# Kernel optimization log

Measured on AMD Instinct MI355X. Metric: run time of the kernel, lower is better.

## Reference

```python
import jax, jax.numpy as jnp
import numpy as np

RADIUS = float(1.5 * 6 * 0.025 / 2.0)  # filter_extent / 2 = 0.1125
N_FLUID, N_BOX, K_F, K_B = 16000, 8000, 64, 32
KS = 4  # kernel size per axis -> 64 bins
EPS = 1e-12


def _radius_neighbors(q, p, radius, K, exclude_self=False):
    Nq = q.shape[0]
    idx = np.zeros((Nq, K), np.int32)
    mask = np.zeros((Nq, K), bool)
    r2 = radius * radius
    kth = min(K, p.shape[0] - 1)
    for s in range(0, Nq, 2048):
        e = min(s + 2048, Nq)
        d2 = ((q[s:e, None, :] - p[None, :, :]) ** 2).sum(-1)
        if exclude_self:
            d2[np.arange(e - s), np.arange(s, e)] = np.inf
        part = np.argpartition(d2, kth, axis=1)[:, :K].astype(np.int32)
        dk = np.take_along_axis(d2, part, 1)
        m = dk <= r2
        part[~m] = 0
        idx[s:e] = part
        mask[s:e] = m
    return idx, mask


def ball_to_cube(d):
    """Volume-preserving map unit ball -> unit cube [-1,1]^3 (Open3D ball_to_cube_volume_preserving)."""
    x, y, z = d[..., 0], d[..., 1], d[..., 2]
    sq = x * x + y * y + z * z
    norm = jnp.sqrt(sq)
    # --- sphere -> cylinder (radius 1, height 2) ---
    xy_sq = x * x + y * y
    polar = (1.25 * z * z) > xy_sq
    s_pol = jnp.sqrt(3.0 * norm / (norm + jnp.abs(z) + EPS))
    s_eq = norm / jnp.sqrt(xy_sq + EPS)
    s = jnp.where(polar, s_pol, s_eq)
    xc = x * s
    yc = y * s
    zc = jnp.where(polar, jnp.sign(z) * norm, 1.5 * z)
    zero = sq < EPS
    xc = jnp.where(zero, 0.0, xc)
    yc = jnp.where(zero, 0.0, yc)
    zc = jnp.where(zero, 0.0, zc)
    # --- cylinder -> cube: inverse Shirley-Chiu concentric map on the xy disc ---
    rxy = jnp.sqrt(xc * xc + yc * yc)
    xbig = jnp.abs(xc) >= jnp.abs(yc)
    safe_x = jnp.where(jnp.abs(xc) > EPS, xc, 1.0)
    safe_y = jnp.where(jnp.abs(yc) > EPS, yc, 1.0)
    four_over_pi = 4.0 / np.pi
    u1 = jnp.sign(xc) * rxy
    v1 = u1 * four_over_pi * jnp.arctan(yc / safe_x)
    v2 = jnp.sign(yc) * rxy
    u2 = v2 * four_over_pi * jnp.arctan(xc / safe_y)
    u = jnp.where(xbig, u1, u2)
    v = jnp.where(xbig, v1, v2)
    zero_xy = rxy < EPS
    u = jnp.where(zero_xy, 0.0, u)
    v = jnp.where(zero_xy, 0.0, v)
    return jnp.stack([u, v, zc], axis=-1)


def cconv(feat_src, pos_src, pos_q, nbr_idx, nbr_mask, filt, bias):
    """ContinuousConv: trilinear (align_corners=True) filter interpolation, poly6 window, no normalization."""
    N = pos_q.shape[0]
    kz, ky, kx, cin, cout = filt.shape
    pj = pos_src[nbr_idx]                       # [N,K,3]
    fj = feat_src[nbr_idx]                      # [N,K,Cin]
    d = (pj - pos_q[:, None, :]) / RADIUS       # normalized offsets in unit ball
    r_sqr = jnp.sum(d * d, axis=-1)             # [N,K]
    win = jnp.clip((1.0 - r_sqr) ** 3, 0.0, 1.0) * nbr_mask.astype(fj.dtype)
    u = ball_to_cube(d)                         # [N,K,3] in [-1,1]
    ks = jnp.asarray([kx, ky, kz], d.dtype)
    g = (u * 0.5 + 0.5) * (ks - 1.0)            # align_corners=True grid coords
    i0 = jnp.clip(jnp.floor(g), 0.0, ks - 2.0).astype(jnp.int32)  # [N,K,3]
    t = g - i0                                  # trilinear fractions
    Fflat = filt.reshape(kz * ky * kx, cin, cout)
    A = jnp.zeros((N, kz * ky * kx, cin), fj.dtype)   # per-query bin accumulator
    n_idx = jnp.arange(N)[:, None]
    for dz in (0, 1):
        for dy in (0, 1):
            for dx in (0, 1):
                w = ((t[..., 0] if dx else 1.0 - t[..., 0])
                     * (t[..., 1] if dy else 1.0 - t[..., 1])
                     * (t[..., 2] if dz else 1.0 - t[..., 2])) * win
                bins = ((i0[..., 2] + dz) * ky + (i0[..., 1] + dy)) * kx + (i0[..., 0] + dx)
                A = A.at[n_idx, bins].add(w[..., None] * fj)
    return jnp.einsum('nbc,bco->no', A, Fflat) + bias


def _forward(pos, vel, box, box_feats,
             w_conv0_fluid, b_conv0_fluid, w_conv0_obstacle, b_conv0_obstacle,
             w_dense0, b_dense0, w_conv1, b_conv1, w_dense1, b_dense1,
             w_conv2, b_conv2, w_dense2, b_dense2,
             nbr_fluid_idx, nbr_fluid_mask, nbr_box_idx, nbr_box_mask):
    fluid_feats = jnp.concatenate([jnp.ones_like(pos[:, :1]), vel], axis=-1)  # [N,4]
    a_cf = cconv(fluid_feats, pos, pos, nbr_fluid_idx, nbr_fluid_mask, w_conv0_fluid, b_conv0_fluid)
    a_df = fluid_feats @ w_dense0 + b_dense0
    a_co = cconv(box_feats, box, pos, nbr_box_idx, nbr_box_mask, w_conv0_obstacle, b_conv0_obstacle)
    feats = jnp.concatenate([a_co, a_cf, a_df], axis=-1)                      # [N,96]
    inp1 = jax.nn.relu(feats)
    ans1 = cconv(inp1, pos, pos, nbr_fluid_idx, nbr_fluid_mask, w_conv1, b_conv1) + inp1 @ w_dense1 + b_dense1
    inp2 = jax.nn.relu(ans1)
    ans2 = (cconv(inp2, pos, pos, nbr_fluid_idx, nbr_fluid_mask, w_conv2, b_conv2)
            + inp2 @ w_dense2 + b_dense2 + ans1)                               # residual (64==64)
    return ans2  # particle_feat = ans_convs[-2] returned by forward()


def setup_inputs() -> dict:
    rng = np.random.default_rng(0)
    L = 1.357  # cube side chosen so avg neighbor count within RADIUS is ~48
    pos = rng.uniform(0, L, (N_FLUID, 3)).astype(np.float32)
    box = rng.uniform(0, L, (N_BOX, 3)).astype(np.float32)
    vel = (0.5 * rng.standard_normal((N_FLUID, 3))).astype(np.float32)
    nrm = rng.standard_normal((N_BOX, 3)).astype(np.float32)
    box_feats = nrm / np.linalg.norm(nrm, axis=-1, keepdims=True)
    nf_idx, nf_mask = _radius_neighbors(pos, pos, RADIUS, K_F, exclude_self=True)
    nb_idx, nb_mask = _radius_neighbors(pos, box, RADIUS, K_B, exclude_self=False)

    def filt(cin, cout):
        s = (6.0 / (cin * KS ** 3 + cout)) ** 0.5
        return (s * rng.standard_normal((KS, KS, KS, cin, cout))).astype(np.float32)

    def lin(cin, cout):
        s = (6.0 / (cin + cout)) ** 0.5
        return (s * rng.standard_normal((cin, cout))).astype(np.float32)

    z = lambda c: np.zeros((c,), np.float32)
    inp = dict(
        pos=pos, vel=vel, box=box, box_feats=box_feats,
        w_conv0_fluid=filt(4, 32), b_conv0_fluid=z(32),
        w_conv0_obstacle=filt(3, 32), b_conv0_obstacle=z(32),
        w_dense0=lin(4, 32), b_dense0=z(32),
        w_conv1=filt(96, 64), b_conv1=z(64), w_dense1=lin(96, 64), b_dense1=z(64),
        w_conv2=filt(64, 64), b_conv2=z(64), w_dense2=lin(64, 64), b_dense2=z(64),
        nbr_fluid_idx=nf_idx, nbr_fluid_mask=nf_mask,
        nbr_box_idx=nb_idx, nbr_box_mask=nb_mask,
    )
    return {k: jnp.asarray(v) for k, v in inp.items()}


def reference(pos, vel, box, box_feats,
              w_conv0_fluid, b_conv0_fluid, w_conv0_obstacle, b_conv0_obstacle,
              w_dense0, b_dense0, w_conv1, b_conv1, w_dense1, b_dense1,
              w_conv2, b_conv2, w_dense2, b_dense2,
              nbr_fluid_idx, nbr_fluid_mask, nbr_box_idx, nbr_box_mask):
    return _forward(pos, vel, box, box_feats,
                    w_conv0_fluid, b_conv0_fluid, w_conv0_obstacle, b_conv0_obstacle,
                    w_dense0, b_dense0, w_conv1, b_conv1, w_dense1, b_dense1,
                    w_conv2, b_conv2, w_dense2, b_dense2,
                    nbr_fluid_idx, nbr_fluid_mask, nbr_box_idx, nbr_box_mask)
```

## Files before the change

### kernel.cpp

```cpp
#include <hip/hip_runtime.h>
#include <cstdint>

#define DEVFN __device__ __forceinline__

using hh8 = __attribute__((ext_vector_type(8))) _Float16;
using f4  = __attribute__((ext_vector_type(4))) float;

constexpr float RAD  = 0.1125f;
constexpr float R2C  = RAD * RAD;
constexpr float EPSF = 1e-12f;
constexpr float FOPI = 1.27323954473516268615f;

DEVFN float sgnf(float a){ return (a > 0.f) ? 1.f : ((a < 0.f) ? -1.f : 0.f); }

DEVFN unsigned short f2h(float f){
  _Float16 h = (_Float16)f;
  union { _Float16 h; unsigned short u; } x; x.h = h; return x.u;
}
DEVFN hh8 ld_hh8(const unsigned short* p){ return *(const hh8*)p; }
DEVFN hh8 ld_b64x2(const unsigned short* p){
  union { unsigned long long q[2]; hh8 v; } u;
  u.q[0] = *(const unsigned long long*)(p);
  u.q[1] = *(const unsigned long long*)(p + 4);
  return u.v;
}

DEVFN void nbr_geom(float ddx, float ddy, float ddz, float factor, int* bins, float* w8)
{
  float x = ddx / RAD, y = ddy / RAD, z = ddz / RAD;
  float sq = x*x + y*y + z*z;
  float omr = 1.f - sq;
  float win = (omr > 0.f) ? omr*omr*omr : 0.f;
  win *= factor;
  float nrm   = sqrtf(sq);
  float xy_sq = x*x + y*y;
  bool  polar = (1.25f*z*z) > xy_sq;
  float s = polar ? sqrtf(3.f*nrm/(nrm + fabsf(z) + EPSF))
                  : (nrm / sqrtf(xy_sq + EPSF));
  float xc = x*s, yc = y*s;
  float zc = polar ? (sgnf(z)*nrm) : (1.5f*z);
  if (sq < EPSF){ xc = 0.f; yc = 0.f; zc = 0.f; }
  float rxy  = sqrtf(xc*xc + yc*yc);
  bool  xbig = fabsf(xc) >= fabsf(yc);
  float sx = (fabsf(xc) > EPSF) ? xc : 1.f;
  float sy = (fabsf(yc) > EPSF) ? yc : 1.f;
  float u1 = sgnf(xc)*rxy;
  float v1 = u1 * FOPI * atanf(yc / sx);
  float v2 = sgnf(yc)*rxy;
  float u2 = v2 * FOPI * atanf(xc / sy);
  float u = xbig ? u1 : u2;
  float v = xbig ? v1 : v2;
  if (rxy < EPSF){ u = 0.f; v = 0.f; }
  float gx = (u *0.5f + 0.5f)*3.f;
  float gy = (v *0.5f + 0.5f)*3.f;
  float gz = (zc*0.5f + 0.5f)*3.f;
  float fx = fminf(fmaxf(floorf(gx), 0.f), 2.f);
  float fy = fminf(fmaxf(floorf(gy), 0.f), 2.f);
  float fz = fminf(fmaxf(floorf(gz), 0.f), 2.f);
  int ix = (int)fx, iy = (int)fy, iz = (int)fz;
  float tx = gx - fx, ty = gy - fy, tz = gz - fz;
  float wx[2] = {1.f - tx, tx};
  float wy[2] = {1.f - ty, ty};
  float wz[2] = {1.f - tz, tz};
  #pragma unroll
  for (int dz2 = 0; dz2 < 2; ++dz2)
    #pragma unroll
    for (int dy2 = 0; dy2 < 2; ++dy2)
      #pragma unroll
      for (int dx2 = 0; dx2 < 2; ++dx2){
        int c = (dz2 << 2) | (dy2 << 1) | dx2;
        bins[c] = ((iz + dz2)*4 + (iy + dy2))*4 + (ix + dx2);
        w8[c]   = wx[dx2]*wy[dy2]*wz[dz2]*win;
      }
}

__global__ __launch_bounds__(256)
void k0_scatter(const float* __restrict__ pos, const float* __restrict__ vel,
                const float* __restrict__ box, const float* __restrict__ boxf,
                const int* __restrict__ nfi, const int* __restrict__ nbi,
                int KB, unsigned short* __restrict__ Abuf)
{
  const int n = blockIdx.x, t = threadIdx.x;
  const int lane = t & 63, w = t >> 6, r = lane & 15, h = lane >> 4;

  __shared__ __align__(16) unsigned short LWf[64*64];
  __shared__ __align__(16) unsigned short LWo[64*32];
  __shared__ __align__(16) unsigned short LBf[16*64];
  __shared__ __align__(16) unsigned short LBo[16*32];
  __shared__ __align__(16) unsigned short Aout[512];
  __shared__ int gjf[64]; __shared__ int gjo[32];

  const float qx = pos[3*n], qy = pos[3*n+1], qz = pos[3*n+2];
  int bins[8]; float w8[8];

  if (w == 0){
    const int k = lane;
    const int j = nfi[(size_t)n*64 + k];
    const float ddx = pos[3*j] - qx, ddy = pos[3*j+1] - qy, ddz = pos[3*j+2] - qz;
    const float d2 = ddx*ddx + ddy*ddy + ddz*ddz;
    unsigned long long zm = __ballot(j == 0);
    int fz = __ffsll(zm) - 1;
    float factor = (j != 0) ? 1.f : ((k == fz && d2 <= R2C && n != 0) ? 1.f : 0.f);
    nbr_geom(ddx, ddy, ddz, factor, bins, w8);
    gjf[k] = j;
  } else if (w == 1){
    const int k = lane;
    const bool act = k < KB;
    const int j = act ? nbi[(size_t)n*KB + k] : 1;
    float ddx = 0.f, ddy = 0.f, ddz = 0.f, d2 = 1e30f;
    if (act){
      ddx = box[3*j] - qx; ddy = box[3*j+1] - qy; ddz = box[3*j+2] - qz;
      d2 = ddx*ddx + ddy*ddy + ddz*ddz;
    }
    unsigned long long zm = __ballot(act && j == 0);
    int fz = __ffsll(zm) - 1;
    float factor = (j != 0) ? 1.f : ((k == fz && d2 <= R2C) ? 1.f : 0.f);
    nbr_geom(ddx, ddy, ddz, factor, bins, w8);
    if (act) gjo[k] = j;
  } else {
    int4 z4 = make_int4(0,0,0,0);
    for (int i = t-128; i < 512; i += 128) *(int4*)&LWf[i*8] = z4;
    for (int i = t-128; i < 256; i += 128) *(int4*)&LWo[i*8] = z4;
    if (t-128 < 128) *(int4*)&LBf[(t-128)*8] = z4;
    if (t-128 <  64) *(int4*)&LBo[(t-128)*8] = z4;
  }
  __syncthreads();

  if (w == 0){
    #pragma unroll
    for (int q = 0; q < 8; ++q){
      int b = bins[q];
      LWf[b*64 + (lane ^ ((b&7)<<3))] = f2h(w8[q]);
    }
  } else if (w == 1){
    if (lane < KB){
      #pragma unroll
      for (int q = 0; q < 8; ++q){
        int b = bins[q];
        LWo[b*32 + (lane ^ ((b&3)<<3))] = f2h(w8[q]);
      }
    }
  } else if (w == 2){
    const int k = lane; const int j = gjf[k];
    LBf[0*64 + k] = f2h(1.f);
    LBf[1*64 + (k ^ 8)]  = f2h(vel[3*j]);
    LBf[2*64 + (k ^ 16)] = f2h(vel[3*j+1]);
    LBf[3*64 + (k ^ 24)] = f2h(vel[3*j+2]);
  } else {
    if (lane < KB){
      const int k = lane; const int j = gjo[k];
      LBo[0*32 + k]        = f2h(boxf[3*j]);
      LBo[1*32 + (k ^ 8)]  = f2h(boxf[3*j+1]);
      LBo[2*32 + (k ^ 16)] = f2h(boxf[3*j+2]);
    }
  }
  __syncthreads();

  f4 aF = {0.f,0.f,0.f,0.f}, aO = {0.f,0.f,0.f,0.f};
  {
    const int b = 16*w + r;
    #pragma unroll
    for (int ks = 0; ks < 2; ++ks){
      hh8 a  = ld_hh8(&LWf[b*64 + (((ks*4+h) ^ (b&7))<<3)]);
      hh8 bb = ld_hh8(&LBf[r*64 + (((ks*4+h) ^ (r&7))<<3)]);
      aF = __builtin_amdgcn_mfma_f32_16x16x32_f16(a, bb, aF, 0,0,0);
    }
    hh8 a2 = ld_hh8(&LWo[b*32 + ((h ^ (b&3))<<3)]);
    hh8 b2 = ld_hh8(&LBo[r*32 + ((h ^ (r&3))<<3)]);
    aO = __builtin_amdgcn_mfma_f32_16x16x32_f16(a2, b2, aO, 0,0,0);
  }
  #pragma unroll
  for (int rr = 0; rr < 4; ++rr){
    int b2 = 16*w + h*4 + rr;
    if (r < 4) Aout[b2*4 + r]       = f2h(aF[rr]);
    if (r < 3) Aout[256 + b2*3 + r] = f2h(aO[rr]);
  }
  if (t == 0){ Aout[448] = f2h(1.f); Aout[452] = f2h(1.f); }
  if (t < 3)   Aout[449 + t] = f2h(vel[3*n + t]);
  if (t < 59)  Aout[453 + t] = 0;
  __syncthreads();

  const int key = n & 7;
  if (t < 64){
    int4 v = *(const int4*)&Aout[t*8];
    *(int4*)&Abuf[(size_t)n*512 + (size_t)(t ^ key)*8] = v;
  }
}

template<int C>
__global__ __launch_bounds__(256)
void k1_scatter(const float* __restrict__ pos, const unsigned short* __restrict__ feat,
                const int* __restrict__ nfi, int n0, unsigned short* __restrict__ Abuf)
{
  constexpr int Kpad = 64*C + C + (C == 96 ? 32 : 0);
  constexpr int CT = C/16;
  constexpr int BTS = 68;
  const int nloc = blockIdx.x;
  const int n = n0 + nloc;
  const int t = threadIdx.x;
  const int lane = t & 63, w = t >> 6, r = lane & 15, h = lane >> 4;

  __shared__ __align__(16) unsigned short sh[4096 + C*BTS];
  unsigned short* W  = sh;
  unsigned short* BT = sh + 4096;
  __shared__ int gj[64];

  int jreg = 0; float qx=0.f,qy=0.f,qz=0.f,px=0.f,py=0.f,pz=0.f;
  if (w == 0){
    jreg = nfi[(size_t)n*64 + lane];
    gj[lane] = jreg;
    qx = pos[3*n]; qy = pos[3*n+1]; qz = pos[3*n+2];
    px = pos[3*jreg]; py = pos[3*jreg+1]; pz = pos[3*jreg+2];
  } else {
    int4 z4 = make_int4(0,0,0,0);
    for (int i = t - 64; i < 512; i += 192) *(int4*)&W[i*8] = z4;
  }
  __syncthreads();

  if (w == 0){
    const int k = lane;
    const float ddx = px - qx, ddy = py - qy, ddz = pz - qz;
    const float d2 = ddx*ddx + ddy*ddy + ddz*ddz;
    unsigned long long zm = __ballot(jreg == 0);
    int fz = __ffsll(zm) - 1;
    float factor = (jreg != 0) ? 1.f : ((k == fz && d2 <= R2C && n != 0) ? 1.f : 0.f);
    int bins[8]; float w8[8];
    nbr_geom(ddx, ddy, ddz, factor, bins, w8);
    #pragma unroll
    for (int q = 0; q < 8; ++q){
      int b = bins[q];
      W[b*64 + (lane ^ ((b&7)<<3))] = f2h(w8[q]);
    }
  } else {
    const int tt = t - 64;
    if constexpr (C == 96){
      const int kb = tt / 48;
      const int cp = tt - kb*48;
      const int c0 = cp*2;
      unsigned short* b0 = BT + c0*BTS;
      unsigned short* b1 = BT + (c0+1)*BTS;
      #pragma unroll 4
      for (int pass = 0; pass < 16; ++pass){
        const int k = pass*4 + kb;
        const int j = gj[k];
        const uint32_t v = *(const uint32_t*)(feat + (size_t)j*96 + c0);
        b0[k] = (unsigned short)(v & 0xffffu);
        b1[k] = (unsigned short)(v >> 16);
      }
    } else {
      const int kb = tt >> 5;
      const int cp = tt & 31;
      const int c0 = cp*2;
      unsigned short* b0 = BT + c0*BTS;
      unsigned short* b1 = BT + (c0+1)*BTS;
      #pragma unroll 4
      for (int pass = 0; pass < 11; ++pass){
        const int k = pass*6 + kb;
        if (k < 64){
          const int j = gj[k];
          const uint32_t v = *(const uint32_t*)(feat + (size_t)j*64 + c0);
          b0[k] = (unsigned short)(v & 0xffffu);
          b1[k] = (unsigned short)(v >> 16);
        }
      }
    }
  }
  __syncthreads();

  f4 acc[CT];
  #pragma unroll
  for (int ct = 0; ct < CT; ++ct) acc[ct] = f4{0.f,0.f,0.f,0.f};
  const int b = 16*w + r;
  #pragma unroll
  for (int ks = 0; ks < 2; ++ks){
    hh8 a = ld_hh8(&W[b*64 + (((ks*4+h) ^ (b&7))<<3)]);
    const int kc = (ks*4 + h)*8;
    #pragma unroll
    for (int ct = 0; ct < CT; ++ct){
      int c = ct*16 + r;
      hh8 bb = ld_b64x2(&BT[c*BTS + kc]);
      acc[ct] = __builtin_amdgcn_mfma_f32_16x16x32_f16(a, bb, acc[ct], 0,0,0);
    }
  }
  __syncthreads();

  unsigned short* Aout = sh;
  #pragma unroll
  for (int ct = 0; ct < CT; ++ct){
    int c = ct*16 + r;
    #pragma unroll
    for (int rr = 0; rr < 4; ++rr){
      int b2 = 16*w + h*4 + rr;
      Aout[b2*C + c] = f2h(acc[ct][rr]);
    }
  }
  if (t < C) Aout[64*C + t] = feat[(size_t)n*C + t];
  if constexpr (C == 96){
    if (t >= 96 && t < 128) Aout[6240 + t - 96] = 0;
  }
  __syncthreads();

  const int key = nloc & 7;
  const size_t rowBase = (size_t)nloc * Kpad;
  for (int ch = t; ch < Kpad/8; ch += 256){
    int4 v = *(const int4*)&Aout[ch*8];
    *(int4*)&Abuf[rowBase + (size_t)(ch ^ key)*8] = v;
  }
}

__global__ __launch_bounds__(256)
void k_bpack(const float* __restrict__ F, const float* __restrict__ Wd,
             int kSplit, int Cd, int Kpad, unsigned short* __restrict__ BpkT)
{
  int idx = blockIdx.x*256 + threadIdx.x;
  int chunks = Kpad/8;
  if (idx >= 64*chunks) return;
  int o = idx / chunks, ch = idx - o*chunks;
  union { int4 v; unsigned short u[8]; } pk;
  #pragma unroll
  for (int e = 0; e < 8; ++e){
    int kp = ch*8 + e;
    float f = 0.f;
    if (kp < kSplit)            f = F[(size_t)kp*64 + o];
    else if (kp < kSplit + Cd)  f = Wd[(size_t)(kp - kSplit)*64 + o];
    pk.u[e] = f2h(f);
  }
  *(int4*)&BpkT[((size_t)o*chunks + (ch ^ (o&7)))*8] = pk.v;
}

__global__ __launch_bounds__(256)
void k_bpack0(const float* __restrict__ Wfilt, const float* __restrict__ Ofilt,
              const float* __restrict__ Wd0, const float* __restrict__ bco,
              const float* __restrict__ bcf, const float* __restrict__ bd0,
              unsigned short* __restrict__ Bpk0)
{
  int idx = blockIdx.x*256 + threadIdx.x;
  if (idx >= 96*64) return;
  int o = idx >> 6, ch = idx & 63;
  union { int4 v; unsigned short u[8]; } pk;
  #pragma unroll
  for (int e = 0; e < 8; ++e){
    int kp = ch*8 + e;
    float f = 0.f;
    if (kp < 256){
      if (o >= 32 && o < 64) f = Wfilt[(size_t)kp*32 + (o - 32)];
    } else if (kp < 448){
      if (o < 32)            f = Ofilt[(size_t)(kp - 256)*32 + o];
    } else if (kp < 452){
      if (o >= 64)           f = Wd0[(size_t)(kp - 448)*32 + (o - 64)];
    } else if (kp == 452){
      f = (o < 32) ? bco[o] : (o < 64) ? bcf[o - 32] : bd0[o - 64];
    }
    pk.u[e] = f2h(f);
  }
  *(int4*)&Bpk0[((size_t)o*64 + (ch ^ (o&7)))*8] = pk.v;
}

template<int NT>
__global__ __launch_bounds__(256)
void k2_gemm(const unsigned short* __restrict__ Abuf, const unsigned short* __restrict__ BpkT,
             float* __restrict__ partial, int n0, int CHa, int Kpad, int ktot,
             int sB, int NF)
{
  const int t = threadIdx.x;
  const int lane = t & 63, w = t >> 6, r = lane & 15, h = lane >> 4;
  const int seg = blockIdx.y;
  const int ks0 = seg*sB;
  const int ks1 = (ks0 + sB < ktot) ? (ks0 + sB) : ktot;
  const int rowBase = blockIdx.x * 128;

  __shared__ __align__(16) unsigned short Asub[128*64];
  __shared__ __align__(16) unsigned short Bsub[16*NT*64];

  f4 acc[2][NT];
  #pragma unroll
  for (int i = 0; i < 2; ++i)
    #pragma unroll
    for (int j = 0; j < NT; ++j) acc[i][j] = f4{0.f,0.f,0.f,0.f};

  for (int ks = ks0; ks < ks1; ++ks){
    #pragma unroll
    for (int i = 0; i < 4; ++i){
      int lin = i*256 + t;
      int row = lin >> 3, lc = lin & 7;
      int grow = rowBase + row; if (grow >= CHa) grow = CHa - 1;
      int4 v = *(const int4*)&Abuf[(size_t)grow*Kpad + ks*64 + lc*8];
      *(int4*)&Asub[lin*8] = v;
    }
    #pragma unroll
    for (int i = 0; i < NT/2; ++i){
      int lin = i*256 + t;
      int o = lin >> 3, lc = lin & 7;
      int4 v = *(const int4*)&BpkT[(size_t)o*Kpad + ks*64 + lc*8];
      *(int4*)&Bsub[lin*8] = v;
    }
    __syncthreads();
    #pragma unroll
    for (int kh = 0; kh < 2; ++kh){
      hh8 a0 = ld_hh8(&Asub[(w*32 +      r)*64 + (((kh*4+h) ^ (r&7))<<3)]);
      hh8 a1 = ld_hh8(&Asub[(w*32 + 16 + r)*64 + (((kh*4+h) ^ (r&7))<<3)]);
      #pragma unroll
      for (int nt = 0; nt < NT; ++nt){
        hh8 bb = ld_hh8(&Bsub[(nt*16 + r)*64 + (((kh*4+h) ^ (r&7))<<3)]);
        acc[0][nt] = __builtin_amdgcn_mfma_f32_16x16x32_f16(a0, bb, acc[0][nt], 0,0,0);
        acc[1][nt] = __builtin_amdgcn_mfma_f32_16x16x32_f16(a1, bb, acc[1][nt], 0,0,0);
      }
    }
    __syncthreads();
  }

  #pragma unroll
  for (int mt = 0; mt < 2; ++mt)
    #pragma unroll
    for (int rr = 0; rr < 4; ++rr){
      int m = rowBase + w*32 + mt*16 + h*4 + rr;
      if (m < CHa){
        float* op = partial + ((size_t)seg*NF + n0 + m)*(16*NT);
        #pragma unroll
        for (int nt = 0; nt < NT; ++nt)
          op[nt*16 + r] = acc[mt][nt][rr];
      }
    }
}

__global__ __launch_bounds__(256)
void k_epi(const float* __restrict__ partial, const float* __restrict__ bc,
           const float* __restrict__ bd, const float* __restrict__ resid,
           float* __restrict__ outRaw, unsigned short* __restrict__ outRelu, int total)
{
  const int i = blockIdx.x*256 + threadIdx.x;
  if (i >= total) return;
  float v = 0.f;
  #pragma unroll
  for (int s = 0; s < 8; ++s) v += partial[(size_t)s*total + i];
  const int o = i & 63;
  v += bc[o] + bd[o];
  if (resid)   v += resid[i];
  if (outRaw)  outRaw[i]  = v;
  if (outRelu) outRelu[i] = f2h(fmaxf(v, 0.f));
}

__global__ __launch_bounds__(256)
void k_epi0(const float* __restrict__ partial, unsigned short* __restrict__ outRelu,
            int total)
{
  const int i = blockIdx.x*256 + threadIdx.x;
  if (i >= total) return;
  float v = 0.f;
  #pragma unroll
  for (int s = 0; s < 4; ++s) v += partial[(size_t)s*total + i];
  outRelu[i] = f2h(fmaxf(v, 0.f));
}

extern "C" void kernel_launch(void* const* d_in, const int* in_sizes, int n_in,
                              void* d_out, int out_size, void* d_ws, size_t ws_size,
                              hipStream_t stream)
{
  const float* pos  = (const float*)d_in[0];
  const float* vel  = (const float*)d_in[1];
  const float* box  = (const float*)d_in[2];
  const float* boxf = (const float*)d_in[3];
  const float* Wc0f = (const float*)d_in[4];
  const float* bc0f = (const float*)d_in[5];
  const float* Wc0o = (const float*)d_in[6];
  const float* bc0o = (const float*)d_in[7];
  const float* Wd0  = (const float*)d_in[8];
  const float* bd0  = (const float*)d_in[9];
  const float* Wc1  = (const float*)d_in[10];
  const float* bc1  = (const float*)d_in[11];
  const float* Wd1  = (const float*)d_in[12];
  const float* bd1  = (const float*)d_in[13];
  const float* Wc2  = (const float*)d_in[14];
  const float* bc2  = (const float*)d_in[15];
  const float* Wd2  = (const float*)d_in[16];
  const float* bd2  = (const float*)d_in[17];
  const int* nfi = (const int*)d_in[18];
  const int* nbi = (const int*)d_in[20];
  const int NF = in_sizes[0]/3;
  const int KB = in_sizes[20]/NF;
  float* out = (float*)d_out;

  char* wsb = (char*)d_ws;
  auto alloc = [&](size_t bytes){ char* p = wsb; wsb += (bytes + 255) & ~(size_t)255; return p; };
  unsigned short* inp1 = (unsigned short*)alloc((size_t)NF*96*2);
  float* ans1    = (float*)alloc((size_t)NF*64*4);
  unsigned short* inp2 = (unsigned short*)alloc((size_t)NF*64*2);
  float* partial = (float*)alloc((size_t)8*NF*64*4);
  unsigned short* Bpk1 = (unsigned short*)alloc((size_t)64*6272*2);
  unsigned short* Bpk2 = (unsigned short*)alloc((size_t)64*4160*2);
  unsigned short* Bpk0 = (unsigned short*)alloc((size_t)96*512*2);
  unsigned short* Abuf = (unsigned short*)wsb;
  size_t usedB = (size_t)(wsb - (char*)d_ws);
  size_t availUS = (ws_size > usedB) ? (ws_size - usedB)/2 : 0;

  auto chunkOf = [&](int Kpad)->int{
    long long c = (long long)(availUS / (size_t)Kpad);
    if (c >= NF) return NF;
    int ch = (int)c & ~127;
    if (ch < 128) ch = 128;
    return ch;
  };

  k_bpack0<<<(96*64 + 255)/256, 256, 0, stream>>>(Wc0f, Wc0o, Wd0, bc0o, bc0f, bd0, Bpk0);
  k_bpack<<<(64*784 + 255)/256, 256, 0, stream>>>(Wc1, Wd1, 6144, 96, 6272, Bpk1);
  k_bpack<<<(64*520 + 255)/256, 256, 0, stream>>>(Wc2, Wd2, 4096, 64, 4160, Bpk2);

  {
    k0_scatter<<<NF, 256, 0, stream>>>(pos, vel, box, boxf, nfi, nbi, KB, Abuf);
    int tiles = (NF + 127)/128;
    k2_gemm<6><<<dim3(tiles, 4), 256, 0, stream>>>(Abuf, Bpk0, partial, 0, NF,
                                                   512, 8, 2, NF);
    k_epi0<<<(NF*96 + 255)/256, 256, 0, stream>>>(partial, inp1, NF*96);
  }
  {
    int CH = chunkOf(6272);
    for (int n0 = 0; n0 < NF; n0 += CH){
      int CHa = (n0 + CH < NF) ? CH : (NF - n0);
      k1_scatter<96><<<CHa, 256, 0, stream>>>(pos, inp1, nfi, n0, Abuf);
      int tiles = (CHa + 127)/128;
      k2_gemm<4><<<dim3(tiles, 8), 256, 0, stream>>>(Abuf, Bpk1, partial, n0, CHa,
                                                     6272, 98, 13, NF);
    }
    k_epi<<<(NF*64 + 255)/256, 256, 0, stream>>>(partial, bc1, bd1, nullptr,
                                                 ans1, inp2, NF*64);
  }
  {
    int CH = chunkOf(4160);
    for (int n0 = 0; n0 < NF; n0 += CH){
      int CHa = (n0 + CH < NF) ? CH : (NF - n0);
      k1_scatter<64><<<CHa, 256, 0, stream>>>(pos, inp2, nfi, n0, Abuf);
      int tiles = (CHa + 127)/128;
      k2_gemm<4><<<dim3(tiles, 8), 256, 0, stream>>>(Abuf, Bpk2, partial, n0, CHa,
                                                     4160, 65, 9, NF);
    }
    k_epi<<<(NF*64 + 255)/256, 256, 0, stream>>>(partial, bc2, bd2, ans1,
                                                 out, nullptr, NF*64);
  }
}
```

Measured before the change: 252.9 us.

## Use direct global-to-LDS loads in GEMM and padded packed scatter layout

The GEMM tile loads now use global_load_lds so A and B data go straight from global memory into LDS, skipping the trip through registers. The scatter kernel swaps the MFMA operand order so each lane writes four packed halves in one 64-bit store, and each bin row is padded (stride 100 or 68) with zero fill. The weight-packing kernel is changed to match the padded K layout. The cost is a larger K dimension (6528/4416 instead of 6272/4160), which adds GEMM work and Abuf traffic.

```diff
diff --git a/kernel.cpp b/kernel.cpp
--- a/kernel.cpp
+++ b/kernel.cpp
@@ -2,6 +2,8 @@
 #include <cstdint>
 
 #define DEVFN __device__ __forceinline__
+#define AS1 __attribute__((address_space(1)))
+#define AS3 __attribute__((address_space(3)))
 
 using hh8 = __attribute__((ext_vector_type(8))) _Float16;
 using f4  = __attribute__((ext_vector_type(4))) float;
@@ -23,6 +25,9 @@
   u.q[0] = *(const unsigned long long*)(p);
   u.q[1] = *(const unsigned long long*)(p + 4);
   return u.v;
+}
+DEVFN void gld16(const void* g, void* l){
+  __builtin_amdgcn_global_load_lds((const AS1 void*)g, (AS3 void*)l, 16, 0, 0);
 }
 
 DEVFN void nbr_geom(float ddx, float ddy, float ddz, float factor, int* bins, float* w8)
@@ -192,7 +197,8 @@
 void k1_scatter(const float* __restrict__ pos, const unsigned short* __restrict__ feat,
                 const int* __restrict__ nfi, int n0, unsigned short* __restrict__ Abuf)
 {
-  constexpr int Kpad = 64*C + C + (C == 96 ? 32 : 0);
+  constexpr int BST  = (C == 96) ? 100 : 68;
+  constexpr int Kpad = (C == 96) ? 6528 : 4416;
   constexpr int CT = C/16;
   constexpr int BTS = 68;
   const int nloc = blockIdx.x;
@@ -279,7 +285,7 @@
     for (int ct = 0; ct < CT; ++ct){
       int c = ct*16 + r;
       hh8 bb = ld_b64x2(&BT[c*BTS + kc]);
-      acc[ct] = __builtin_amdgcn_mfma_f32_16x16x32_f16(a, bb, acc[ct], 0,0,0);
+      acc[ct] = __builtin_amdgcn_mfma_f32_16x16x32_f16(bb, a, acc[ct], 0,0,0);
     }
   }
   __syncthreads();
@@ -287,17 +293,19 @@
   unsigned short* Aout = sh;
   #pragma unroll
   for (int ct = 0; ct < CT; ++ct){
-    int c = ct*16 + r;
-    #pragma unroll
-    for (int rr = 0; rr < 4; ++rr){
-      int b2 = 16*w + h*4 + rr;
-      Aout[b2*C + c] = f2h(acc[ct][rr]);
-    }
-  }
-  if (t < C) Aout[64*C + t] = feat[(size_t)n*C + t];
+    unsigned long long pk =
+        (unsigned long long)f2h(acc[ct][0])
+      | ((unsigned long long)f2h(acc[ct][1]) << 16)
+      | ((unsigned long long)f2h(acc[ct][2]) << 32)
+      | ((unsigned long long)f2h(acc[ct][3]) << 48);
+    const int c0 = ct*16 + h*4;
+    *(unsigned long long*)&Aout[b*BST + c0] = pk;
+  }
+  Aout[(t >> 2)*BST + C + (t & 3)] = 0;
   if constexpr (C == 96){
-    if (t >= 96 && t < 128) Aout[6240 + t - 96] = 0;
-  }
+    if (t < 32) Aout[6496 + t] = 0;
+  }
+  if (t < C) Aout[64*BST + t] = feat[(size_t)n*C + t];
   __syncthreads();
 
   const int key = nloc & 7;
@@ -310,19 +318,24 @@
 
 __global__ __launch_bounds__(256)
 void k_bpack(const float* __restrict__ F, const float* __restrict__ Wd,
-             int kSplit, int Cd, int Kpad, unsigned short* __restrict__ BpkT)
+             int Cin, int BST, int Cd, int Kpad, unsigned short* __restrict__ BpkT)
 {
   int idx = blockIdx.x*256 + threadIdx.x;
   int chunks = Kpad/8;
   if (idx >= 64*chunks) return;
   int o = idx / chunks, ch = idx - o*chunks;
+  const int kDense = 64*BST;
   union { int4 v; unsigned short u[8]; } pk;
   #pragma unroll
   for (int e = 0; e < 8; ++e){
     int kp = ch*8 + e;
     float f = 0.f;
-    if (kp < kSplit)            f = F[(size_t)kp*64 + o];
-    else if (kp < kSplit + Cd)  f = Wd[(size_t)(kp - kSplit)*64 + o];
+    if (kp < kDense){
+      int bin = kp / BST, c = kp - bin*BST;
+      if (c < Cin) f = F[((size_t)bin*Cin + c)*64 + o];
+    } else if (kp < kDense + Cd){
+      f = Wd[(size_t)(kp - kDense)*64 + o];
+    }
     pk.u[e] = f2h(f);
   }
   *(int4*)&BpkT[((size_t)o*chunks + (ch ^ (o&7)))*8] = pk.v;
@@ -364,6 +377,7 @@
 {
   const int t = threadIdx.x;
   const int lane = t & 63, w = t >> 6, r = lane & 15, h = lane >> 4;
+  const int wbase = t & ~63;
   const int seg = blockIdx.y;
   const int ks0 = seg*sB;
   const int ks1 = (ks0 + sB < ktot) ? (ks0 + sB) : ktot;
@@ -384,15 +398,15 @@
       int lin = i*256 + t;
       int row = lin >> 3, lc = lin & 7;
       int grow = rowBase + row; if (grow >= CHa) grow = CHa - 1;
-      int4 v = *(const int4*)&Abuf[(size_t)grow*Kpad + ks*64 + lc*8];
-      *(int4*)&Asub[lin*8] = v;
+      gld16(&Abuf[(size_t)grow*Kpad + ks*64 + lc*8],
+            &Asub[(size_t)(i*256 + wbase)*8]);
     }
     #pragma unroll
     for (int i = 0; i < NT/2; ++i){
       int lin = i*256 + t;
       int o = lin >> 3, lc = lin & 7;
-      int4 v = *(const int4*)&BpkT[(size_t)o*Kpad + ks*64 + lc*8];
-      *(int4*)&Bsub[lin*8] = v;
+      gld16(&BpkT[(size_t)o*Kpad + ks*64 + lc*8],
+            &Bsub[(size_t)(i*256 + wbase)*8]);
     }
     __syncthreads();
     #pragma unroll
@@ -480,14 +494,16 @@
   const int KB = in_sizes[20]/NF;
   float* out = (float*)d_out;
 
+  const int Kp1 = 6528, Kp2 = 4416;
+
   char* wsb = (char*)d_ws;
   auto alloc = [&](size_t bytes){ char* p = wsb; wsb += (bytes + 255) & ~(size_t)255; return p; };
   unsigned short* inp1 = (unsigned short*)alloc((size_t)NF*96*2);
   float* ans1    = (float*)alloc((size_t)NF*64*4);
   unsigned short* inp2 = (unsigned short*)alloc((size_t)NF*64*2);
   float* partial = (float*)alloc((size_t)8*NF*64*4);
-  unsigned short* Bpk1 = (unsigned short*)alloc((size_t)64*6272*2);
-  unsigned short* Bpk2 = (unsigned short*)alloc((size_t)64*4160*2);
+  unsigned short* Bpk1 = (unsigned short*)alloc((size_t)64*Kp1*2);
+  unsigned short* Bpk2 = (unsigned short*)alloc((size_t)64*Kp2*2);
   unsigned short* Bpk0 = (unsigned short*)alloc((size_t)96*512*2);
   unsigned short* Abuf = (unsigned short*)wsb;
   size_t usedB = (size_t)(wsb - (char*)d_ws);
@@ -502,8 +518,8 @@
   };
 
   k_bpack0<<<(96*64 + 255)/256, 256, 0, stream>>>(Wc0f, Wc0o, Wd0, bc0o, bc0f, bd0, Bpk0);
-  k_bpack<<<(64*784 + 255)/256, 256, 0, stream>>>(Wc1, Wd1, 6144, 96, 6272, Bpk1);
-  k_bpack<<<(64*520 + 255)/256, 256, 0, stream>>>(Wc2, Wd2, 4096, 64, 4160, Bpk2);
+  k_bpack<<<(64*(Kp1/8) + 255)/256, 256, 0, stream>>>(Wc1, Wd1, 96, 100, 96, Kp1, Bpk1);
+  k_bpack<<<(64*(Kp2/8) + 255)/256, 256, 0, stream>>>(Wc2, Wd2, 64,  68, 64, Kp2, Bpk2);
 
   {
     k0_scatter<<<NF, 256, 0, stream>>>(pos, vel, box, boxf, nfi, nbi, KB, Abuf);
@@ -513,25 +529,25 @@
     k_epi0<<<(NF*96 + 255)/256, 256, 0, stream>>>(partial, inp1, NF*96);
   }
   {
-    int CH = chunkOf(6272);
+    int CH = chunkOf(Kp1);
     for (int n0 = 0; n0 < NF; n0 += CH){
       int CHa = (n0 + CH < NF) ? CH : (NF - n0);
       k1_scatter<96><<<CHa, 256, 0, stream>>>(pos, inp1, nfi, n0, Abuf);
       int tiles = (CHa + 127)/128;
       k2_gemm<4><<<dim3(tiles, 8), 256, 0, stream>>>(Abuf, Bpk1, partial, n0, CHa,
-                                                     6272, 98, 13, NF);
+                                                     Kp1, Kp1/64, 13, NF);
     }
     k_epi<<<(NF*64 + 255)/256, 256, 0, stream>>>(partial, bc1, bd1, nullptr,
                                                  ans1, inp2, NF*64);
   }
   {
-    int CH = chunkOf(4160);
+    int CH = chunkOf(Kp2);
     for (int n0 = 0; n0 < NF; n0 += CH){
       int CHa = (n0 + CH < NF) ? CH : (NF - n0);
       k1_scatter<64><<<CHa, 256, 0, stream>>>(pos, inp2, nfi, n0, Abuf);
       int tiles = (CHa + 127)/128;
       k2_gemm<4><<<dim3(tiles, 8), 256, 0, stream>>>(Abuf, Bpk2, partial, n0, CHa,
-                                                     4160, 65, 9, NF);
+                                                     Kp2, Kp2/64, 9, NF);
     }
     k_epi<<<(NF*64 + 255)/256, 256, 0, stream>>>(partial, bc2, bd2, ans1,
                                                  out, nullptr, NF*64);
```

New measurement: 250.8 us. No clear change (-0.8%).
